# Performance work log

Measured on AMD Instinct MI355X. Metric: run time of the kernel, lower is better.

Reference implementation:

```python
import jax, jax.numpy as jnp
import numpy as np

V, E, H, L = 100, 128, 256, 64   # vocab, embed, hidden, latent
B, T = 4096, 128                 # batch, seq_len


def setup_inputs() -> dict:
    key = jax.random.key(0)
    ks = jax.random.split(key, 20)
    s = 0.05
    def rn(k, shape):
        return jax.random.normal(k, shape, dtype=jnp.float32) * s
    return {
        "x": jax.random.randint(ks[0], (B, T), 0, V, dtype=jnp.int32),
        "eps": jax.random.normal(ks[1], (B, L), dtype=jnp.float32),
        "embedding": rn(ks[2], (V, E)),
        "enc_Wih": rn(ks[3], (3 * H, E)),
        "enc_Whh": rn(ks[4], (3 * H, H)),
        "enc_bih": rn(ks[5], (3 * H,)),
        "enc_bhh": rn(ks[6], (3 * H,)),
        "mu_W": rn(ks[7], (L, H)),
        "mu_b": rn(ks[8], (L,)),
        "lv_W": rn(ks[9], (L, H)),
        "lv_b": rn(ks[10], (L,)),
        "di_W": rn(ks[11], (H, L)),
        "di_b": rn(ks[12], (H,)),
        "dec_Wih": rn(ks[13], (3 * H, L)),
        "dec_Whh": rn(ks[14], (3 * H, H)),
        "dec_bih": rn(ks[15], (3 * H,)),
        "dec_bhh": rn(ks[16], (3 * H,)),
        "out_W": rn(ks[17], (V, H)),
        "out_b": rn(ks[18], (V,)),
    }


def _gru_step(h, x_proj, W_hh, b_hh):
    # PyTorch GRU gate semantics. x_proj = W_ih @ x + b_ih precomputed.
    hp = h @ W_hh.T + b_hh                       # [B, 3H]
    xr, xz, xn = jnp.split(x_proj, 3, axis=-1)
    hr, hz, hn = jnp.split(hp, 3, axis=-1)
    r = jax.nn.sigmoid(xr + hr)
    zg = jax.nn.sigmoid(xz + hz)
    n = jnp.tanh(xn + r * hn)
    return (1.0 - zg) * n + zg * h


def reference(x, eps, embedding, enc_Wih, enc_Whh, enc_bih, enc_bhh,
              mu_W, mu_b, lv_W, lv_b, di_W, di_b,
              dec_Wih, dec_Whh, dec_bih, dec_bhh, out_W, out_b):
    # ---- encode ----
    emb = embedding[x]                                        # [B, T, E]
    # Precompute input projections for all timesteps at once.
    x_proj = jnp.einsum('bte,ge->btg', emb, enc_Wih) + enc_bih  # [B, T, 3H]
    h0 = jnp.zeros((x.shape[0], H), dtype=emb.dtype)

    def enc_body(h, xp_t):
        h = _gru_step(h, xp_t, enc_Whh, enc_bhh)
        return h, None

    h_last, _ = jax.lax.scan(enc_body, h0, jnp.swapaxes(x_proj, 0, 1))
    mu = h_last @ mu_W.T + mu_b                               # [B, L]
    logvar = h_last @ lv_W.T + lv_b                           # [B, L]

    # ---- reparameterize ----
    z = mu + eps * jnp.exp(0.5 * logvar)                      # [B, L]

    # ---- decode (same z fed as input every step, as in the original) ----
    hidden = jnp.tanh(z @ di_W.T + di_b)                      # [B, H]
    zp = z @ dec_Wih.T + dec_bih                              # [B, 3H], constant per step

    def dec_body(h, _):
        h = _gru_step(h, zp, dec_Whh, dec_bhh)
        return h, h

    max_len = x.shape[1]
    _, hs = jax.lax.scan(dec_body, hidden, None, length=max_len)  # [T, B, H]
    logits = jnp.einsum('tbh,vh->btv', hs, out_W) + out_b         # [B, T, V]
    return logits, mu, logvar
```

## Files before the change

### kernel.cpp

```cpp
#include <hip/hip_runtime.h>
#include <hip/hip_bf16.h>

#define VOCAB 100
#define EDIM  128
#define HDIM  256
#define LDIM  64
#define G3    768
#define TT    128
#define BB    4096
#define LROW  (TT * VOCAB)
#define H_LD  264
#define ZP_LD 17

typedef float    f32x4 __attribute__((ext_vector_type(4)));
typedef _Float16 f16x8 __attribute__((ext_vector_type(8)));
typedef _Float16 f16x4 __attribute__((ext_vector_type(4)));

__device__ __forceinline__ float sigf(float x) {
    return __builtin_amdgcn_rcpf(1.0f + __expf(-x));
}
__device__ __forceinline__ float tanh_f(float x) {
    return 2.0f * __builtin_amdgcn_rcpf(1.0f + __expf(-2.0f * x)) - 1.0f;
}
__device__ __forceinline__ void barrier_lgkm() {
    asm volatile("s_waitcnt lgkmcnt(0)\n\ts_barrier" ::: "memory");
}

__device__ __forceinline__ f16x8 ld_bfrag(const float* __restrict__ W, int outcol, int ks, int lgrp) {
    const float* p = W + outcol * HDIM + ks * 32 + lgrp * 8;
    float4 a = *(const float4*)p;
    float4 b = *(const float4*)(p + 4);
    f16x8 w = {(_Float16)a.x, (_Float16)a.y, (_Float16)a.z, (_Float16)a.w,
               (_Float16)b.x, (_Float16)b.y, (_Float16)b.z, (_Float16)b.w};
    return w;
}

__global__ void pt_kernel(const float* __restrict__ emb, const float* __restrict__ Wih,
                          const float* __restrict__ bih, const float* __restrict__ bhh,
                          _Float16* __restrict__ PT) {
    int v = blockIdx.x;
    __shared__ float se[EDIM];
    for (int e = threadIdx.x; e < EDIM; e += blockDim.x) se[e] = emb[v * EDIM + e];
    __syncthreads();
    for (int g = threadIdx.x; g < G3; g += blockDim.x) {
        const float* wr = Wih + g * EDIM;
        float acc = bih[g] + (g < 512 ? bhh[g] : 0.0f);
        #pragma unroll 8
        for (int e = 0; e < EDIM; ++e) acc += se[e] * wr[e];
        PT[v * G3 + g] = (_Float16)acc;
    }
}

__global__ __launch_bounds__(1024, 4) void enc_kernel(
    const int* __restrict__ x, const _Float16* __restrict__ PT2,
    const float* __restrict__ Whh, const float* __restrict__ bhh,
    float* __restrict__ out)
{
    __shared__ _Float16 s_h[2][16 * H_LD];
    __shared__ int s_tok[16 * TT];

    const int tid  = threadIdx.x;
    const int lane = tid & 63;
    const int wv   = tid >> 6;
    const int l15  = lane & 15;
    const int lgrp = lane >> 4;
    const int bbase = blockIdx.x * 16;
    const int col  = wv * 16 + l15;

    for (int i = tid; i < 16 * TT; i += 1024) s_tok[i] = x[bbase * TT + i];

    f16x8 Breg[3][8];
    #pragma unroll
    for (int g = 0; g < 3; ++g)
        #pragma unroll
        for (int ks = 0; ks < 8; ++ks)
            Breg[g][ks] = ld_bfrag(Whh, g * 256 + col, ks, lgrp);

    const float bhn = bhh[512 + col];
    float hst[4] = {0.f, 0.f, 0.f, 0.f};

    for (int i = tid; i < 16 * H_LD; i += 1024) s_h[0][i] = (_Float16)0.f;
    __syncthreads();

    int tokp[4];
    #pragma unroll
    for (int j = 0; j < 4; ++j) tokp[j] = s_tok[(lgrp * 4 + j) * TT];

    const f32x4 z4 = {0.f, 0.f, 0.f, 0.f};

    #pragma unroll 1
    for (int t = 0; t < TT; ++t) {
        const _Float16* rh = s_h[t & 1];
        _Float16* wh = s_h[(t + 1) & 1];

        _Float16 pr[4], pz[4], pn[4];
        #pragma unroll
        for (int j = 0; j < 4; ++j) {
            const _Float16* p = PT2 + tokp[j] * G3 + col;
            pr[j] = p[0]; pz[j] = p[256]; pn[j] = p[512];
        }

        f32x4 a0 = z4, a1 = z4, a2 = z4;
        #pragma unroll
        for (int ks = 0; ks < 8; ++ks) {
            f16x8 a = *(const f16x8*)(rh + l15 * H_LD + ks * 32 + lgrp * 8);
            a0 = __builtin_amdgcn_mfma_f32_16x16x32_f16(a, Breg[0][ks], a0, 0, 0, 0);
            a1 = __builtin_amdgcn_mfma_f32_16x16x32_f16(a, Breg[1][ks], a1, 0, 0, 0);
            a2 = __builtin_amdgcn_mfma_f32_16x16x32_f16(a, Breg[2][ks], a2, 0, 0, 0);
        }

        if (t + 1 < TT) {
            #pragma unroll
            for (int j = 0; j < 4; ++j) tokp[j] = s_tok[(lgrp * 4 + j) * TT + t + 1];
        }

        #pragma unroll
        for (int j = 0; j < 4; ++j) {
            const int row = lgrp * 4 + j;
            float rg = sigf(a0[j] + (float)pr[j]);
            float zg = sigf(a1[j] + (float)pz[j]);
            float n  = tanh_f((float)pn[j] + rg * (a2[j] + bhn));
            float h  = n + zg * (hst[j] - n);
            hst[j] = h;
            wh[row * H_LD + col] = (_Float16)h;
            if (t == TT - 1) out[(size_t)(bbase + row) * LROW + col] = h;
        }
        barrier_lgkm();
    }
}

__global__ __launch_bounds__(512, 2) void mid_kernel(
    const float* __restrict__ eps,
    const float* __restrict__ mu_W, const float* __restrict__ mu_b,
    const float* __restrict__ lv_W, const float* __restrict__ lv_b,
    const float* __restrict__ di_W, const float* __restrict__ di_b,
    const float* __restrict__ dec_Wih, const float* __restrict__ dec_bih,
    const float* __restrict__ dec_bhh,
    float* __restrict__ out, f16x4* __restrict__ zq_g, float* __restrict__ h0_g)
{
    __shared__ float s_hl[16 * 260];

    const int tid  = threadIdx.x;
    const int bbase = blockIdx.x * 16;

    for (int i = tid; i < 16 * HDIM; i += 512) {
        int m = i >> 8, c = i & 255;
        s_hl[m * 260 + c] = out[(size_t)(bbase + m) * LROW + c];
    }
    __syncthreads();

    float z0 = 0.f, z1 = 0.f;
    {
        const size_t MU_OFF = (size_t)BB * TT * VOCAB;
        const size_t LV_OFF = MU_OFF + (size_t)BB * LDIM;
        #pragma unroll
        for (int oo = 0; oo < 2; ++oo) {
            int o = tid * 2 + oo;
            int m = o >> 6, j = o & 63;
            const float* mwr = mu_W + j * HDIM;
            const float* lwr = lv_W + j * HDIM;
            float am = mu_b[j], al = lv_b[j];
            #pragma unroll 4
            for (int k = 0; k < HDIM; ++k) { float hv = s_hl[m * 260 + k]; am += hv * mwr[k]; al += hv * lwr[k]; }
            size_t bo = (size_t)(bbase + m) * LDIM + j;
            out[MU_OFF + bo] = am;
            out[LV_OFF + bo] = al;
            float zv = am + eps[bo] * __expf(0.5f * al);
            if (oo == 0) z0 = zv; else z1 = zv;
        }
    }
    __syncthreads();
    {
        int o0 = tid * 2;
        s_hl[(o0 >> 6) * 260 + (o0 & 63)] = z0;
        int o1 = o0 + 1;
        s_hl[(o1 >> 6) * 260 + (o1 & 63)] = z1;
    }
    __syncthreads();

    {
        const int gc = tid & 255;
        const int gm2 = tid >> 8;
        float ah[8], ar[8], az[8], an[8];
        float dib = di_b[gc];
        float bir = dec_bih[gc], biz = dec_bih[gc + 256], bin_ = dec_bih[gc + 512];
        #pragma unroll
        for (int i = 0; i < 8; ++i) { ah[i] = dib; ar[i] = bir; az[i] = biz; an[i] = bin_; }
        const float* w0 = di_W + gc * LDIM;
        const float* w1 = dec_Wih + gc * LDIM;
        const float* w2 = dec_Wih + (gc + 256) * LDIM;
        const float* w3 = dec_Wih + (gc + 512) * LDIM;
        #pragma unroll 2
        for (int j = 0; j < LDIM; ++j) {
            float a0 = w0[j], a1 = w1[j], a2 = w2[j], a3 = w3[j];
            #pragma unroll
            for (int i = 0; i < 8; ++i) {
                float q = s_hl[(gm2 + 2 * i) * 260 + j];
                ah[i] += q * a0; ar[i] += q * a1; az[i] += q * a2; an[i] += q * a3;
            }
        }
        float bhr = dec_bhh[gc], bhz = dec_bhh[gc + 256], bhn_c = dec_bhh[gc + 512];
        #pragma unroll
        for (int i = 0; i < 8; ++i) {
            int m = gm2 + 2 * i;
            float th = tanh_f(ah[i]);
            h0_g[(size_t)(bbase + m) * 256 + gc] = th;
            f16x4 q = {(_Float16)(ar[i] + bhr), (_Float16)(az[i] + bhz), (_Float16)an[i], (_Float16)bhn_c};
            zq_g[(size_t)(bbase + m) * 256 + gc] = q;
        }
    }
}

__global__ __launch_bounds__(1024, 4) void dec_rnn_kernel(
    const float* __restrict__ dec_Whh,
    const f16x4* __restrict__ zq_g, const float* __restrict__ h0_g,
    _Float16* __restrict__ Hbuf)
{
    __shared__ _Float16 s_hb[2][16 * H_LD];
    __shared__ f16x4 s_zq[256 * ZP_LD];

    const int tid  = threadIdx.x;
    const int lane = tid & 63;
    const int wv   = tid >> 6;
    const int l15  = lane & 15;
    const int lgrp = lane >> 4;
    const int bbase = blockIdx.x * 16;
    const int col  = wv * 16 + l15;

    for (int i = tid; i < 16 * HDIM; i += 1024) {
        int row = i >> 8, c = i & 255;
        float hv = h0_g[(size_t)(bbase + row) * 256 + c];
        s_hb[0][row * H_LD + c] = (_Float16)hv;
        s_zq[c * ZP_LD + row] = zq_g[(size_t)(bbase + row) * 256 + c];
    }

    f16x8 Breg[3][8];
    #pragma unroll
    for (int g = 0; g < 3; ++g)
        #pragma unroll
        for (int ks = 0; ks < 8; ++ks)
            Breg[g][ks] = ld_bfrag(dec_Whh, g * 256 + col, ks, lgrp);

    float hst[4];
    #pragma unroll
    for (int j = 0; j < 4; ++j)
        hst[j] = h0_g[(size_t)(bbase + lgrp * 4 + j) * 256 + col];
    __syncthreads();

    const f32x4 z4 = {0.f, 0.f, 0.f, 0.f};
    const int crow = tid >> 6;
    const int cseg = lane;
    _Float16* hb = Hbuf + ((size_t)(bbase + crow) * TT) * 256 + cseg * 4;
    const int lread = crow * H_LD + cseg * 4;

    #pragma unroll 1
    for (int t = 0; t < TT; ++t) {
        const _Float16* rh = s_hb[t & 1];
        _Float16* wh = s_hb[(t + 1) & 1];

        f32x4 a0 = z4, a1 = z4, a2 = z4;
        #pragma unroll
        for (int ks = 0; ks < 8; ++ks) {
            f16x8 a = *(const f16x8*)(rh + l15 * H_LD + ks * 32 + lgrp * 8);
            a0 = __builtin_amdgcn_mfma_f32_16x16x32_f16(a, Breg[0][ks], a0, 0, 0, 0);
            a1 = __builtin_amdgcn_mfma_f32_16x16x32_f16(a, Breg[1][ks], a1, 0, 0, 0);
            a2 = __builtin_amdgcn_mfma_f32_16x16x32_f16(a, Breg[2][ks], a2, 0, 0, 0);
        }
        #pragma unroll
        for (int j = 0; j < 4; ++j) {
            const int row = lgrp * 4 + j;
            f16x4 q = s_zq[col * ZP_LD + row];
            float rg = sigf(a0[j] + (float)q[0]);
            float zg = sigf(a1[j] + (float)q[1]);
            float n  = tanh_f((float)q[2] + rg * (a2[j] + (float)q[3]));
            float h  = n + zg * (hst[j] - n);
            hst[j] = h;
            wh[row * H_LD + col] = (_Float16)h;
        }
        barrier_lgkm();
        *(f16x4*)hb = *(const f16x4*)(wh + lread);
        hb += 256;
    }
}

__global__ __launch_bounds__(1024, 4) void logits_kernel(
    const _Float16* __restrict__ Hbuf, const float* __restrict__ out_W,
    const float* __restrict__ out_b, float* __restrict__ out)
{
    __shared__ __attribute__((aligned(16))) unsigned char s_outw[VOCAB * 512];
    __shared__ __attribute__((aligned(16))) float s_ls[256 * 108];
    const int tid = threadIdx.x, lane = tid & 63, wv = tid >> 6;
    const int l15 = lane & 15, lgrp = lane >> 4;

    for (int idx = tid; idx < VOCAB * HDIM; idx += 1024) {
        int r = idx >> 8, k = idx & 255;
        _Float16 w = (_Float16)out_W[r * 256 + k];
        *(short*)(s_outw + r * 512 + ((2 * k) ^ ((r & 7) << 4))) = __builtin_bit_cast(short, w);
    }
    __syncthreads();

    float ob[7];
    #pragma unroll
    for (int vt = 0; vt < 7; ++vt) {
        int v = vt * 16 + l15;
        ob[vt] = (v < VOCAB) ? out_b[v] : 0.0f;
    }
    const f32x4 z4 = {0.f, 0.f, 0.f, 0.f};

    #pragma unroll 1
    for (int round = 0; round < 2; ++round) {
        size_t mt = (size_t)blockIdx.x * 32 + round * 16 + wv;
        const _Float16* hrow = Hbuf + (mt * 16 + l15) * 256;
        f32x4 acc[7];
        #pragma unroll
        for (int vt = 0; vt < 7; ++vt) acc[vt] = z4;
        #pragma unroll
        for (int ks = 0; ks < 8; ++ks) {
            f16x8 a = *(const f16x8*)(hrow + ks * 32 + lgrp * 8);
            #pragma unroll
            for (int vt = 0; vt < 7; ++vt) {
                int orow = vt * 16 + l15; if (orow > VOCAB - 1) orow = VOCAB - 1;
                f16x8 wo = *(const f16x8*)(s_outw + orow * 512 + ((ks * 64 + lgrp * 16) ^ ((orow & 7) << 4)));
                acc[vt] = __builtin_amdgcn_mfma_f32_16x16x32_f16(a, wo, acc[vt], 0, 0, 0);
            }
        }
        #pragma unroll
        for (int vt = 0; vt < 7; ++vt) {
            int v = vt * 16 + l15;
            if (v < VOCAB) {
                #pragma unroll
                for (int j = 0; j < 4; ++j)
                    s_ls[(wv * 16 + lgrp * 4 + j) * 108 + v] = acc[vt][j] + ob[vt];
            }
        }
        __syncthreads();
        {
            size_t slabM0 = (size_t)blockIdx.x * 512 + round * 256;
            float* gbase = out + slabM0 * VOCAB;
            for (int c = tid; c < 6400; c += 1024) {
                int r = c / 25, cc = (c % 25) * 4;
                f32x4 vch = *(const f32x4*)(s_ls + r * 108 + cc);
                *(f32x4*)(gbase + (size_t)c * 4) = vch;
            }
        }
        __syncthreads();
    }
}

__global__ __launch_bounds__(1024, 4) void dec_fused_kernel(
    const float* __restrict__ eps,
    const float* __restrict__ mu_W, const float* __restrict__ mu_b,
    const float* __restrict__ lv_W, const float* __restrict__ lv_b,
    const float* __restrict__ di_W, const float* __restrict__ di_b,
    const float* __restrict__ dec_Wih, const float* __restrict__ dec_Whh,
    const float* __restrict__ dec_bih, const float* __restrict__ dec_bhh,
    const float* __restrict__ out_W, const float* __restrict__ out_b,
    float* __restrict__ out)
{
    __shared__ _Float16 s_hb[2][16 * H_LD];
    __shared__ f16x4 s_zp[256 * ZP_LD];
    __shared__ __attribute__((aligned(16))) unsigned char s_outw[VOCAB * 512];
    __shared__ float s_hl[16 * 260];

    const int tid  = threadIdx.x;
    const int lane = tid & 63;
    const int wv   = tid >> 6;
    const int l15  = lane & 15;
    const int lgrp = lane >> 4;
    const int bbase = blockIdx.x * 16;
    const int col  = wv * 16 + l15;

    for (int i = tid; i < 16 * HDIM; i += 1024) {
        int m = i >> 8, c = i & 255;
        s_hl[m * 260 + c] = out[(size_t)(bbase + m) * LROW + c];
    }
    for (int idx = tid; idx < VOCAB * HDIM; idx += 1024) {
        int r = idx >> 8, k = idx & 255;
        _Float16 w = (_Float16)out_W[r * 256 + k];
        *(short*)(s_outw + r * 512 + ((2 * k) ^ ((r & 7) << 4))) = __builtin_bit_cast(short, w);
    }

    f16x8 Breg[3][8];
    #pragma unroll
    for (int g = 0; g < 3; ++g)
        #pragma unroll
        for (int ks = 0; ks < 8; ++ks)
            Breg[g][ks] = ld_bfrag(dec_Whh, g * 256 + col, ks, lgrp);
    __syncthreads();

    float zv;
    {
        const size_t MU_OFF = (size_t)BB * TT * VOCAB;
        const size_t LV_OFF = MU_OFF + (size_t)BB * LDIM;
        int m = tid >> 6, j = tid & 63;
        const float* mwr = mu_W + j * HDIM;
        const float* lwr = lv_W + j * HDIM;
        float am = mu_b[j], al = lv_b[j];
        #pragma unroll 4
        for (int k = 0; k < HDIM; ++k) { float hv = s_hl[m * 260 + k]; am += hv * mwr[k]; al += hv * lwr[k]; }
        size_t bo = (size_t)(bbase + m) * LDIM + j;
        out[MU_OFF + bo] = am;
        out[LV_OFF + bo] = al;
        zv = am + eps[bo] * __expf(0.5f * al);
    }
    __syncthreads();
    { int m = tid >> 6, j = tid & 63; s_hl[m * 260 + j] = zv; }
    __syncthreads();

    float th[4];
    {
        const int gc = tid & 255;
        const int gm = tid >> 8;
        float ah[4], ar[4], az[4], an[4];
        float dib = di_b[gc];
        float bir = dec_bih[gc], biz = dec_bih[gc + 256], bin_ = dec_bih[gc + 512];
        #pragma unroll
        for (int i = 0; i < 4; ++i) { ah[i] = dib; ar[i] = bir; az[i] = biz; an[i] = bin_; }
        const float* w0 = di_W + gc * LDIM;
        const float* w1 = dec_Wih + gc * LDIM;
        const float* w2 = dec_Wih + (gc + 256) * LDIM;
        const float* w3 = dec_Wih + (gc + 512) * LDIM;
        #pragma unroll 2
        for (int j = 0; j < LDIM; ++j) {
            float a0 = w0[j], a1 = w1[j], a2 = w2[j], a3 = w3[j];
            #pragma unroll
            for (int i = 0; i < 4; ++i) {
                float q = s_hl[(gm * 4 + i) * 260 + j];
                ah[i] += q * a0; ar[i] += q * a1; az[i] += q * a2; an[i] += q * a3;
            }
        }
        float bhr = dec_bhh[gc], bhz = dec_bhh[gc + 256];
        __syncthreads();
        #pragma unroll
        for (int i = 0; i < 4; ++i) {
            int r = gm * 4 + i;
            th[i] = tanh_f(ah[i]);
            s_hl[r * 260 + gc] = th[i];
            f16x4 q = {(_Float16)(ar[i] + bhr), (_Float16)(az[i] + bhz), (_Float16)an[i], (_Float16)0.f};
            s_zp[gc * ZP_LD + r] = q;
            s_hb[0][r * H_LD + gc] = (_Float16)th[i];
        }
    }
    __syncthreads();

    float hpr[4];
    #pragma unroll
    for (int j = 0; j < 4; ++j) hpr[j] = s_hl[(lgrp * 4 + j) * 260 + col];

    const float bhn = dec_bhh[512 + col];
    const int vcol = wv * 16 + l15;
    const int orow = (vcol < VOCAB) ? vcol : (VOCAB - 1);
    const float ob = (wv < 7 && vcol < VOCAB) ? out_b[vcol] : 0.0f;
    const f32x4 z4 = {0.f, 0.f, 0.f, 0.f};

    #pragma unroll 1
    for (int t = 0; t < TT; ++t) {
        const _Float16* rh = s_hb[t & 1];
        _Float16* wh = s_hb[(t + 1) & 1];

        f32x4 a0 = z4, a1 = z4, a2 = z4, aco = z4;
        #pragma unroll
        for (int ks = 0; ks < 8; ++ks) {
            f16x8 a = *(const f16x8*)(rh + l15 * H_LD + ks * 32 + lgrp * 8);
            a0 = __builtin_amdgcn_mfma_f32_16x16x32_f16(a, Breg[0][ks], a0, 0, 0, 0);
            a1 = __builtin_amdgcn_mfma_f32_16x16x32_f16(a, Breg[1][ks], a1, 0, 0, 0);
            a2 = __builtin_amdgcn_mfma_f32_16x16x32_f16(a, Breg[2][ks], a2, 0, 0, 0);
            if (wv < 7) {
                f16x8 wo = *(const f16x8*)(s_outw + orow * 512 + ((ks * 64 + lgrp * 16) ^ ((orow & 7) << 4)));
                aco = __builtin_amdgcn_mfma_f32_16x16x32_f16(a, wo, aco, 0, 0, 0);
            }
        }
        if (t > 0 && wv < 7 && vcol < VOCAB) {
            size_t base = (size_t)(bbase + lgrp * 4) * LROW + (size_t)(t - 1) * VOCAB + vcol;
            #pragma unroll
            for (int j = 0; j < 4; ++j) out[base + (size_t)j * LROW] = aco[j] + ob;
        }
        #pragma unroll
        for (int j = 0; j < 4; ++j) {
            const int row = lgrp * 4 + j;
            f16x4 q = s_zp[col * ZP_LD + lgrp * 4 + j];
            float rg = sigf(a0[j] + (float)q[0]);
            float zg = sigf(a1[j] + (float)q[1]);
            float n  = tanh_f((float)q[2] + rg * (a2[j] + bhn));
            float h  = n + zg * (hpr[j] - n);
            hpr[j] = h;
            wh[row * H_LD + col] = (_Float16)h;
        }
        barrier_lgkm();
    }

    if (wv < 7) {
        const _Float16* rh = s_hb[0];
        f32x4 aco = z4;
        #pragma unroll
        for (int ks = 0; ks < 8; ++ks) {
            f16x8 a  = *(const f16x8*)(rh + l15 * H_LD + ks * 32 + lgrp * 8);
            f16x8 wo = *(const f16x8*)(s_outw + orow * 512 + ((ks * 64 + lgrp * 16) ^ ((orow & 7) << 4)));
            aco = __builtin_amdgcn_mfma_f32_16x16x32_f16(a, wo, aco, 0, 0, 0);
        }
        if (vcol < VOCAB) {
            size_t base = (size_t)(bbase + lgrp * 4) * LROW + (size_t)(TT - 1) * VOCAB + vcol;
            #pragma unroll
            for (int j = 0; j < 4; ++j) out[base + (size_t)j * LROW] = aco[j] + ob;
        }
    }
}

extern "C" void kernel_launch(void* const* d_in, const int* in_sizes, int n_in,
                              void* d_out, int out_size, void* d_ws, size_t ws_size,
                              hipStream_t stream) {
    const int*   x       = (const int*)  d_in[0];
    const float* eps     = (const float*)d_in[1];
    const float* emb     = (const float*)d_in[2];
    const float* enc_Wih = (const float*)d_in[3];
    const float* enc_Whh = (const float*)d_in[4];
    const float* enc_bih = (const float*)d_in[5];
    const float* enc_bhh = (const float*)d_in[6];
    const float* mu_W    = (const float*)d_in[7];
    const float* mu_b    = (const float*)d_in[8];
    const float* lv_W    = (const float*)d_in[9];
    const float* lv_b    = (const float*)d_in[10];
    const float* di_W    = (const float*)d_in[11];
    const float* di_b    = (const float*)d_in[12];
    const float* dec_Wih = (const float*)d_in[13];
    const float* dec_Whh = (const float*)d_in[14];
    const float* dec_bih = (const float*)d_in[15];
    const float* dec_bhh = (const float*)d_in[16];
    const float* out_W   = (const float*)d_in[17];
    const float* out_b   = (const float*)d_in[18];
    float* out = (float*)d_out;

    _Float16* PT = (_Float16*)d_ws;
    const size_t ZQ_OFF = 153600;
    const size_t H0_OFF = ZQ_OFF + (size_t)BB * 256 * 8;
    const size_t HB_OFF = H0_OFF + (size_t)BB * 256 * 4;
    f16x4*    zq_g = (f16x4*)((char*)d_ws + ZQ_OFF);
    float*    h0_g = (float*)((char*)d_ws + H0_OFF);
    _Float16* Hbuf = (_Float16*)((char*)d_ws + HB_OFF);
    const size_t need = HB_OFF + (size_t)BB * TT * 256 * sizeof(_Float16);

    pt_kernel<<<VOCAB, 256, 0, stream>>>(emb, enc_Wih, enc_bih, enc_bhh, PT);
    enc_kernel<<<BB / 16, 1024, 0, stream>>>(x, PT, enc_Whh, enc_bhh, out);
    if (ws_size >= need) {
        mid_kernel<<<BB / 16, 512, 0, stream>>>(eps, mu_W, mu_b, lv_W, lv_b,
            di_W, di_b, dec_Wih, dec_bih, dec_bhh, out, zq_g, h0_g);
        dec_rnn_kernel<<<BB / 16, 1024, 0, stream>>>(dec_Whh, zq_g, h0_g, Hbuf);
        logits_kernel<<<(BB * TT / 16) / 32, 1024, 0, stream>>>(Hbuf, out_W, out_b, out);
    } else {
        dec_fused_kernel<<<BB / 16, 1024, 0, stream>>>(eps, mu_W, mu_b, lv_W, lv_b,
            di_W, di_b, dec_Wih, dec_Whh, dec_bih, dec_bhh, out_W, out_b, out);
    }
}
```

Before: 860.4 us.

## Halve encoder block to 512 threads with two column groups per wave and packed tables

The encoder GRU kernel now uses 8 waves per block, each computing 32 hidden columns (two 16-column MFMA tiles), so every A-fragment LDS read feeds six MFMAs instead of three. The weight fragments are loaded with a K-permuted layout so each lane's two output columns are adjacent, which lets it pack them into one 32-bit LDS store. The token projection table is repacked as f16x4 (r,z,n,bhn) per column for a single vector gather. The cost is doubled register use for the weights (48 f16x8 fragments per lane) and fewer waves per block, which may reduce occupancy and latency hiding.

```diff
diff --git a/kernel.cpp b/kernel.cpp
--- a/kernel.cpp
+++ b/kernel.cpp
@@ -25,6 +25,9 @@
 __device__ __forceinline__ void barrier_lgkm() {
     asm volatile("s_waitcnt lgkmcnt(0)\n\ts_barrier" ::: "memory");
 }
+__device__ __forceinline__ unsigned short h2b(_Float16 h) {
+    return __builtin_bit_cast(unsigned short, h);
+}
 
 __device__ __forceinline__ f16x8 ld_bfrag(const float* __restrict__ W, int outcol, int ks, int lgrp) {
     const float* p = W + outcol * HDIM + ks * 32 + lgrp * 8;
@@ -35,25 +38,41 @@
     return w;
 }
 
+__device__ __forceinline__ f16x8 ld_bfragK(const float* __restrict__ W, int outcol, int ks, int lgrp) {
+    const float* p = W + outcol * HDIM + ks * 32 + lgrp * 4;
+    float4 f0 = *(const float4*)p;
+    float4 f1 = *(const float4*)(p + 16);
+    f16x8 w = {(_Float16)f0.x, (_Float16)f1.x, (_Float16)f0.y, (_Float16)f1.y,
+               (_Float16)f0.z, (_Float16)f1.z, (_Float16)f0.w, (_Float16)f1.w};
+    return w;
+}
+
 __global__ void pt_kernel(const float* __restrict__ emb, const float* __restrict__ Wih,
                           const float* __restrict__ bih, const float* __restrict__ bhh,
-                          _Float16* __restrict__ PT) {
+                          f16x4* __restrict__ PT) {
     int v = blockIdx.x;
+    int col = threadIdx.x;
     __shared__ float se[EDIM];
-    for (int e = threadIdx.x; e < EDIM; e += blockDim.x) se[e] = emb[v * EDIM + e];
-    __syncthreads();
-    for (int g = threadIdx.x; g < G3; g += blockDim.x) {
-        const float* wr = Wih + g * EDIM;
-        float acc = bih[g] + (g < 512 ? bhh[g] : 0.0f);
-        #pragma unroll 8
-        for (int e = 0; e < EDIM; ++e) acc += se[e] * wr[e];
-        PT[v * G3 + g] = (_Float16)acc;
-    }
-}
-
-__global__ __launch_bounds__(1024, 4) void enc_kernel(
-    const int* __restrict__ x, const _Float16* __restrict__ PT2,
-    const float* __restrict__ Whh, const float* __restrict__ bhh,
+    if (col < EDIM) se[col] = emb[v * EDIM + col];
+    __syncthreads();
+    const float* wr = Wih + col * EDIM;
+    const float* wz = Wih + (col + 256) * EDIM;
+    const float* wn = Wih + (col + 512) * EDIM;
+    float xr = bih[col]       + bhh[col];
+    float xz = bih[col + 256] + bhh[col + 256];
+    float xn = bih[col + 512];
+    #pragma unroll 4
+    for (int e = 0; e < EDIM; ++e) {
+        float s = se[e];
+        xr += s * wr[e]; xz += s * wz[e]; xn += s * wn[e];
+    }
+    f16x4 q = {(_Float16)xr, (_Float16)xz, (_Float16)xn, (_Float16)bhh[512 + col]};
+    PT[v * 256 + col] = q;
+}
+
+__global__ __launch_bounds__(512, 2) void enc_kernel(
+    const int* __restrict__ x, const f16x4* __restrict__ PT3,
+    const float* __restrict__ Whh,
     float* __restrict__ out)
 {
     __shared__ _Float16 s_h[2][16 * H_LD];
@@ -65,21 +84,24 @@
     const int l15  = lane & 15;
     const int lgrp = lane >> 4;
     const int bbase = blockIdx.x * 16;
-    const int col  = wv * 16 + l15;
-
-    for (int i = tid; i < 16 * TT; i += 1024) s_tok[i] = x[bbase * TT + i];
-
-    f16x8 Breg[3][8];
+    const int colb = wv * 32 + l15;
+
+    for (int i = tid; i < 16 * TT; i += 512) s_tok[i] = x[bbase * TT + i];
+
+    f16x8 Breg[3][2][8];
     #pragma unroll
     for (int g = 0; g < 3; ++g)
         #pragma unroll
-        for (int ks = 0; ks < 8; ++ks)
-            Breg[g][ks] = ld_bfrag(Whh, g * 256 + col, ks, lgrp);
-
-    const float bhn = bhh[512 + col];
-    float hst[4] = {0.f, 0.f, 0.f, 0.f};
-
-    for (int i = tid; i < 16 * H_LD; i += 1024) s_h[0][i] = (_Float16)0.f;
+        for (int cg = 0; cg < 2; ++cg)
+            #pragma unroll
+            for (int ks = 0; ks < 8; ++ks)
+                Breg[g][cg][ks] = ld_bfragK(Whh, g * 256 + colb + cg * 16, ks, lgrp);
+
+    float hst[4][2];
+    #pragma unroll
+    for (int j = 0; j < 4; ++j) { hst[j][0] = 0.f; hst[j][1] = 0.f; }
+
+    for (int i = tid; i < 16 * H_LD; i += 512) s_h[0][i] = (_Float16)0.f;
     __syncthreads();
 
     int tokp[4];
@@ -93,20 +115,25 @@
         const _Float16* rh = s_h[t & 1];
         _Float16* wh = s_h[(t + 1) & 1];
 
-        _Float16 pr[4], pz[4], pn[4];
+        f16x4 q[4][2];
         #pragma unroll
         for (int j = 0; j < 4; ++j) {
-            const _Float16* p = PT2 + tokp[j] * G3 + col;
-            pr[j] = p[0]; pz[j] = p[256]; pn[j] = p[512];
-        }
-
-        f32x4 a0 = z4, a1 = z4, a2 = z4;
+            const f16x4* p = PT3 + tokp[j] * 256 + colb;
+            q[j][0] = p[0];
+            q[j][1] = p[16];
+        }
+
+        f32x4 acc[3][2];
+        #pragma unroll
+        for (int g = 0; g < 3; ++g) { acc[g][0] = z4; acc[g][1] = z4; }
         #pragma unroll
         for (int ks = 0; ks < 8; ++ks) {
             f16x8 a = *(const f16x8*)(rh + l15 * H_LD + ks * 32 + lgrp * 8);
-            a0 = __builtin_amdgcn_mfma_f32_16x16x32_f16(a, Breg[0][ks], a0, 0, 0, 0);
-            a1 = __builtin_amdgcn_mfma_f32_16x16x32_f16(a, Breg[1][ks], a1, 0, 0, 0);
-            a2 = __builtin_amdgcn_mfma_f32_16x16x32_f16(a, Breg[2][ks], a2, 0, 0, 0);
+            #pragma unroll
+            for (int g = 0; g < 3; ++g) {
+                acc[g][0] = __builtin_amdgcn_mfma_f32_16x16x32_f16(a, Breg[g][0][ks], acc[g][0], 0, 0, 0);
+                acc[g][1] = __builtin_amdgcn_mfma_f32_16x16x32_f16(a, Breg[g][1][ks], acc[g][1], 0, 0, 0);
+            }
         }
 
         if (t + 1 < TT) {
@@ -117,13 +144,19 @@
         #pragma unroll
         for (int j = 0; j < 4; ++j) {
             const int row = lgrp * 4 + j;
-            float rg = sigf(a0[j] + (float)pr[j]);
-            float zg = sigf(a1[j] + (float)pz[j]);
-            float n  = tanh_f((float)pn[j] + rg * (a2[j] + bhn));
-            float h  = n + zg * (hst[j] - n);
-            hst[j] = h;
-            wh[row * H_LD + col] = (_Float16)h;
-            if (t == TT - 1) out[(size_t)(bbase + row) * LROW + col] = h;
+            unsigned wpack = 0;
+            #pragma unroll
+            for (int cg = 0; cg < 2; ++cg) {
+                f16x4 qq = q[j][cg];
+                float rg = sigf(acc[0][cg][j] + (float)qq[0]);
+                float zg = sigf(acc[1][cg][j] + (float)qq[1]);
+                float n  = tanh_f((float)qq[2] + rg * (acc[2][cg][j] + (float)qq[3]));
+                float h  = n + zg * (hst[j][cg] - n);
+                hst[j][cg] = h;
+                if (t == TT - 1) out[(size_t)(bbase + row) * LROW + colb + cg * 16] = h;
+                wpack |= ((unsigned)h2b((_Float16)h)) << (16 * cg);
+            }
+            *(unsigned*)(wh + row * H_LD + wv * 32 + 2 * l15) = wpack;
         }
         barrier_lgkm();
     }
@@ -530,8 +563,8 @@
     const float* out_b   = (const float*)d_in[18];
     float* out = (float*)d_out;
 
-    _Float16* PT = (_Float16*)d_ws;
-    const size_t ZQ_OFF = 153600;
+    f16x4* PT3 = (f16x4*)d_ws;
+    const size_t ZQ_OFF = 204800;
     const size_t H0_OFF = ZQ_OFF + (size_t)BB * 256 * 8;
     const size_t HB_OFF = H0_OFF + (size_t)BB * 256 * 4;
     f16x4*    zq_g = (f16x4*)((char*)d_ws + ZQ_OFF);
@@ -539,8 +572,8 @@
     _Float16* Hbuf = (_Float16*)((char*)d_ws + HB_OFF);
     const size_t need = HB_OFF + (size_t)BB * TT * 256 * sizeof(_Float16);
 
-    pt_kernel<<<VOCAB, 256, 0, stream>>>(emb, enc_Wih, enc_bih, enc_bhh, PT);
-    enc_kernel<<<BB / 16, 1024, 0, stream>>>(x, PT, enc_Whh, enc_bhh, out);
+    pt_kernel<<<VOCAB, 256, 0, stream>>>(emb, enc_Wih, enc_bih, enc_bhh, PT3);
+    enc_kernel<<<BB / 16, 512, 0, stream>>>(x, PT3, enc_Whh, out);
     if (ws_size >= need) {
         mid_kernel<<<BB / 16, 512, 0, stream>>>(eps, mu_W, mu_b, lv_W, lv_b,
             di_W, di_b, dec_Wih, dec_bih, dec_bhh, out, zq_g, h0_g);
```

Result: faster. 811.3 us (-5.7%).
